# Performance work log

Measured on AMD Instinct MI355X. Metric: run time of the kernel, lower is better.

## Reference

```python
import jax, jax.numpy as jnp
import numpy as np

D_MODEL = 1024
NHEAD = 16
HEAD_DIM = D_MODEL // NHEAD


def setup_inputs() -> dict:
    key = jax.random.key(0)
    ks = jax.random.split(key, 9)
    B, T = 2, 2048
    s = 1.0 / np.sqrt(D_MODEL)
    return {
        "sequence": jax.random.normal(ks[0], (B, T, D_MODEL), dtype=jnp.float32),
        "wq": jax.random.normal(ks[1], (D_MODEL, D_MODEL), dtype=jnp.float32) * s,
        "bq": jax.random.normal(ks[2], (D_MODEL,), dtype=jnp.float32) * 0.01,
        "wk": jax.random.normal(ks[3], (D_MODEL, D_MODEL), dtype=jnp.float32) * s,
        "bk": jax.random.normal(ks[4], (D_MODEL,), dtype=jnp.float32) * 0.01,
        "wv": jax.random.normal(ks[5], (D_MODEL, D_MODEL), dtype=jnp.float32) * s,
        "bv": jax.random.normal(ks[6], (D_MODEL,), dtype=jnp.float32) * 0.01,
        "wo": jax.random.normal(ks[7], (D_MODEL, D_MODEL), dtype=jnp.float32) * s,
        "bo": jax.random.normal(ks[8], (D_MODEL,), dtype=jnp.float32) * 0.01,
    }


def reference(sequence, wq, bq, wk, bk, wv, bv, wo, bo):
    B, T, C = sequence.shape
    scale = jnp.asarray(HEAD_DIM ** 0.5, sequence.dtype)
    # projections (nn.Linear: x @ W.T + b)
    def proj(x, w, b):
        y = x @ w.T + b
        return y.reshape(B, T, NHEAD, HEAD_DIM).transpose(0, 2, 1, 3)  # [B,H,T,Dh]
    q = proj(sequence, wq, bq)
    k = proj(sequence, wk, bk)
    v = proj(sequence, wv, bv)
    scores = jnp.einsum("bhqd,bhkd->bhqk", q, k) / scale
    causal = jnp.tril(jnp.ones((T, T), dtype=bool))
    scores = jnp.where(causal, scores, jnp.asarray(-jnp.inf, scores.dtype))
    attn = jax.nn.softmax(scores, axis=-1)
    out = jnp.einsum("bhqk,bhkd->bhqd", attn, v)
    out = out.transpose(0, 2, 1, 3).reshape(B, T, C)
    return out @ wo.T + bo
```

## Files before the change

kernel.cpp:

```cpp
#include <hip/hip_runtime.h>
#include <hip/hip_bf16.h>
#include <hip/hip_fp16.h>
#include <type_traits>

#define DM 1024
#define NH 16
#define HD 64
#define BATCH 2
#define SEQ 2048
#define MROWS (BATCH*SEQ)

typedef __hip_bfloat16 bf16;
typedef __attribute__((ext_vector_type(8))) short    bf16x8;
typedef __attribute__((ext_vector_type(8))) short    s16x8;
typedef __attribute__((ext_vector_type(8))) _Float16 f16x8;
typedef __attribute__((ext_vector_type(4))) _Float16 f16x4;
typedef __attribute__((ext_vector_type(4))) short    s16x4;
typedef __attribute__((ext_vector_type(4))) float    f32x4;

#define LOG2E 1.44269504f
#define M_FIX 4.0f

__device__ __forceinline__ short f2bf(float x) {
    union { float f; unsigned u; } v; v.f = x;
    unsigned r = v.u + 0x7FFF + ((v.u >> 16) & 1);
    return (short)(r >> 16);
}

__device__ __forceinline__ bf16x8 ld8f(const float* p) {
    const float4 a = *(const float4*)p;
    const float4 b = *(const float4*)(p + 4);
    bf16x8 r;
    r[0]=f2bf(a.x); r[1]=f2bf(a.y); r[2]=f2bf(a.z); r[3]=f2bf(a.w);
    r[4]=f2bf(b.x); r[5]=f2bf(b.y); r[6]=f2bf(b.z); r[7]=f2bf(b.w);
    return r;
}

__device__ __forceinline__ void gload_lds16(const void* g, void* l) {
    __builtin_amdgcn_global_load_lds(
        (const __attribute__((address_space(1))) void*)g,
        (__attribute__((address_space(3))) void*)l, 16, 0, 0);
}

__global__ __launch_bounds__(256)
void cvt_bf16(const float* __restrict__ s0, const float* __restrict__ s1,
              const float* __restrict__ s2, const float* __restrict__ s3,
              const float* __restrict__ s4,
              short* d0, short* d1, short* d2, short* d3, short* d4)
{
    const int y = blockIdx.y;
    const float* src = (y==0? s0 : y==1? s1 : y==2? s2 : y==3? s3 : s4);
    short*       dst = (y==0? d0 : y==1? d1 : y==2? d2 : y==3? d3 : d4);
    const int n = (y == 0) ? MROWS*DM : DM*DM;
    const int i = (blockIdx.x * 256 + threadIdx.x) * 8;
    if (i < n) *(bf16x8*)(dst + i) = ld8f(src + i);
}

template<int MODE>
__device__ __forceinline__
void gemm_epilogue(f32x4 (&acc)[4][4], const float* bi, void* out, int z,
                   int tile_m, int tile_n, int wm, int wn,
                   int fr, int quad, int lane, short* lA)
{
    if (MODE == 1 && z == 2) {
        __syncthreads();
        short* sc = lA + (int)(threadIdx.x >> 6) * 256;
        const int rd = lane >> 2, tc = lane & 3;
        #pragma unroll
        for (int mi = 0; mi < 4; ++mi) {
            #pragma unroll
            for (int ni = 0; ni < 4; ++ni) {
                const int colg = tile_n + wn + ni*16 + fr;
                const float bia = bi[colg];
                f16x4 w;
                #pragma unroll
                for (int r = 0; r < 4; ++r) w[r] = (_Float16)(acc[mi][ni][r] + bia);
                *(f16x4*)(sc + fr*16 + quad*4) = w;
                const f16x4 vv = *(const f16x4*)(sc + rd*16 + tc*4);
                const int dg = tile_n + wn + ni*16 + rd;
                const int tg = tile_m + wm + mi*16 + tc*4;
                const int hh = dg >> 6, dd = dg & (HD-1);
                const int bb = tg >> 11, tt = tg & (SEQ-1);
                const int kt = tt >> 5, tko = tt & 31;
                *(f16x4*)((_Float16*)out +
                    ((((size_t)(bb*NH + hh))*(SEQ/32) + kt)*HD + dd)*32 + tko) = vv;
            }
        }
    } else {
        #pragma unroll
        for (int mi = 0; mi < 4; ++mi) {
            #pragma unroll
            for (int ni = 0; ni < 4; ++ni) {
                const int colg = tile_n + wn + ni*16 + fr;
                const float bia = bi[colg];
                #pragma unroll
                for (int r = 0; r < 4; ++r) {
                    const int rowg = tile_m + wm + mi*16 + quad*4 + r;
                    const float v = acc[mi][ni][r] + bia;
                    if (MODE == 0) {
                        ((float*)out)[(size_t)rowg*DM + colg] = v;
                    } else {
                        const int bb = rowg >> 11, t = rowg & (SEQ-1);
                        const int h  = colg >> 6,  d = colg & (HD-1);
                        ((_Float16*)out)[(((size_t)(bb*NH + h))*SEQ + t)*HD + d] = (_Float16)v;
                    }
                }
            }
        }
    }
}

template<int MODE>
__global__ __launch_bounds__(256)
void gemm_a(const short* __restrict__ A,
            const short* __restrict__ W0, const short* __restrict__ W1, const short* __restrict__ W2,
            const float* __restrict__ b0, const float* __restrict__ b1, const float* __restrict__ b2,
            void* o0, void* o1, void* o2)
{
    __shared__ __align__(16) short lA[128*32];
    __shared__ __align__(16) short lB[128*32];

    const int tid  = threadIdx.x;
    const int wid  = tid >> 6;
    const int lane = tid & 63;
    const int tile_n = blockIdx.x * 128;
    const int tile_m = blockIdx.y * 128;
    const int z = blockIdx.z;

    const short* Wg = (z == 0 ? W0 : (z == 1 ? W1 : W2));
    const float* bi = (z == 0 ? b0 : (z == 1 ? b1 : b2));
    void*        out = (z == 0 ? o0 : (z == 1 ? o1 : o2));

    const int sa_row = tile_m + wid*32 + (lane >> 2);
    const int sb_row = tile_n + wid*32 + (lane >> 2);
    const int scol   = (lane & 3) * 8;
    short* lA0 = lA + wid*1024 + lane*8;
    short* lA1 = lA0 + 512;
    short* lB0 = lB + wid*1024 + lane*8;
    short* lB1 = lB0 + 512;

    const int wm = (wid >> 1) * 64;
    const int wn = (wid & 1) * 64;
    const int fr = lane & 15;
    const int quad = lane >> 4;
    const int fq = quad * 8;

    f32x4 acc[4][4] = {};

    for (int k0 = 0; k0 < DM; k0 += 32) {
        __syncthreads();
        gload_lds16(A  + (size_t)sa_row*DM      + k0 + scol, lA0);
        gload_lds16(A  + (size_t)(sa_row+16)*DM + k0 + scol, lA1);
        gload_lds16(Wg + (size_t)sb_row*DM      + k0 + scol, lB0);
        gload_lds16(Wg + (size_t)(sb_row+16)*DM + k0 + scol, lB1);
        __syncthreads();

        bf16x8 af[4], bfv[4];
        #pragma unroll
        for (int i = 0; i < 4; ++i) af[i]  = *(const bf16x8*)(lA + (wm + i*16 + fr)*32 + fq);
        #pragma unroll
        for (int i = 0; i < 4; ++i) bfv[i] = *(const bf16x8*)(lB + (wn + i*16 + fr)*32 + fq);

        #pragma unroll
        for (int mi = 0; mi < 4; ++mi)
            #pragma unroll
            for (int ni = 0; ni < 4; ++ni)
                acc[mi][ni] = __builtin_amdgcn_mfma_f32_16x16x32_bf16(
                    af[mi], bfv[ni], acc[mi][ni], 0, 0, 0);
    }
    gemm_epilogue<MODE>(acc, bi, out, z, tile_m, tile_n, wm, wn, fr, quad, lane, lA);
}

template<typename TA, int MODE>
__global__ __launch_bounds__(256)
void gemm_f(const TA* __restrict__ A,
            const float* __restrict__ W0, const float* __restrict__ W1, const float* __restrict__ W2,
            const float* __restrict__ b0, const float* __restrict__ b1, const float* __restrict__ b2,
            void* o0, void* o1, void* o2)
{
    __shared__ __align__(16) short lA[128*32];
    __shared__ __align__(16) short lB[128*32];

    const int tid  = threadIdx.x;
    const int wid  = tid >> 6;
    const int lane = tid & 63;
    const int tile_n = blockIdx.x * 128;
    const int tile_m = blockIdx.y * 128;
    const int z = blockIdx.z;

    const float* Wg = (z == 0 ? W0 : (z == 1 ? W1 : W2));
    const float* bi = (z == 0 ? b0 : (z == 1 ? b1 : b2));
    void*        out = (z == 0 ? o0 : (z == 1 ? o1 : o2));

    const int sa_row = tile_m + wid*32 + (lane >> 2);
    const int sb_row = tile_n + wid*32 + (lane >> 2);
    const int scol   = (lane & 3) * 8;
    short* lA0 = lA + wid*1024 + lane*8;
    short* lA1 = lA0 + 512;
    short* lB0 = lB + wid*1024 + lane*8;
    short* lB1 = lB0 + 512;

    const int wm = (wid >> 1) * 64;
    const int wn = (wid & 1) * 64;
    const int fr = lane & 15;
    const int quad = lane >> 4;
    const int fq = quad * 8;

    f32x4 acc[4][4] = {};

    for (int k0 = 0; k0 < DM; k0 += 32) {
        bf16x8 ra0, ra1;
        if constexpr (std::is_same<TA, float>::value) {
            ra0 = ld8f((const float*)A + (size_t)sa_row*DM      + k0 + scol);
            ra1 = ld8f((const float*)A + (size_t)(sa_row+16)*DM + k0 + scol);
        } else {
            ra0 = *(const bf16x8*)((const short*)A + (size_t)sa_row*DM      + k0 + scol);
            ra1 = *(const bf16x8*)((const short*)A + (size_t)(sa_row+16)*DM + k0 + scol);
        }
        const bf16x8 rb0 = ld8f(Wg + (size_t)sb_row*DM      + k0 + scol);
        const bf16x8 rb1 = ld8f(Wg + (size_t)(sb_row+16)*DM + k0 + scol);

        __syncthreads();
        *(bf16x8*)lA0 = ra0;
        *(bf16x8*)lA1 = ra1;
        *(bf16x8*)lB0 = rb0;
        *(bf16x8*)lB1 = rb1;
        __syncthreads();

        bf16x8 af[4], bfv[4];
        #pragma unroll
        for (int i = 0; i < 4; ++i) af[i]  = *(const bf16x8*)(lA + (wm + i*16 + fr)*32 + fq);
        #pragma unroll
        for (int i = 0; i < 4; ++i) bfv[i] = *(const bf16x8*)(lB + (wn + i*16 + fr)*32 + fq);

        #pragma unroll
        for (int mi = 0; mi < 4; ++mi)
            #pragma unroll
            for (int ni = 0; ni < 4; ++ni)
                acc[mi][ni] = __builtin_amdgcn_mfma_f32_16x16x32_bf16(
                    af[mi], bfv[ni], acc[mi][ni], 0, 0, 0);
    }
    gemm_epilogue<MODE>(acc, bi, out, z, tile_m, tile_n, wm, wn, fr, quad, lane, lA);
}

__global__ __launch_bounds__(512)
void attn(const _Float16* __restrict__ Q, const _Float16* __restrict__ K,
          const _Float16* __restrict__ Vt, short* __restrict__ O)
{
    __shared__ __align__(16) _Float16 lsK[2][2][2048];
    __shared__ __align__(16) _Float16 lsV[2][2][2048];
    __shared__ __align__(16) float    comb[64*68];
    __shared__ float                  lcomb[64];

    const int t    = threadIdx.x;
    const int lane = t & 63;
    const int wid  = t >> 6;
    const int wg   = wid >> 2;
    const int widl = wid & 3;
    const int tg   = t & 255;
    const int id   = blockIdx.x;
    const int bh   = id & 31;
    const int xb   = id >> 5;
    const size_t base = (size_t)bh * SEQ * HD;
    const int qr = lane & 15;
    const int quad = lane >> 4;
    const int bb = bh >> 4, h = bh & (NH-1);

    const int k_goff = ((tg>>2)&31)*64 + (tg>>7)*32 + (tg&3)*8;
    const int v_goff = (tg&63)*32 + (tg>>6)*8;

    const float SC1 = 0.125f * LOG2E;
    const float SC2 = -M_FIX * LOG2E;
    const int vboff = (quad>>1)*512 + (quad&1)*4 + qr*8;

    #pragma unroll 1
    for (int half = 0; half < 2; ++half) {
        const int band = half ? (31 - xb) : xb;
        const int q_tile = band*64 + widl*16;
        const int q_idx  = q_tile + qr;
        const int nsub   = band + 1;
        const int k0sub  = wg * nsub;
        const int ktm    = 2*band + (widl >> 1);

        const f16x8* Qv = (const f16x8*)(Q + base + (size_t)q_idx*HD);
        const f16x8 qf0 = Qv[quad];
        const f16x8 qf1 = Qv[quad + 4];

        float l_cur = 0.f;
        f32x4 o[4] = {};

        gload_lds16(K  + base + (size_t)k0sub*2048 + k_goff, &lsK[wg][0][0] + tg*8);
        gload_lds16(Vt + base + (size_t)k0sub*2048 + v_goff, &lsV[wg][0][0] + tg*8);

        int cur = 0;
        #pragma unroll 1
        for (int u = 0; u < nsub; ++u) {
            if (u + 1 < nsub) {
                const size_t g = base + (size_t)(k0sub + u + 1)*2048;
                gload_lds16(K  + g + k_goff, &lsK[wg][cur^1][0] + tg*8);
                gload_lds16(Vt + g + v_goff, &lsV[wg][cur^1][0] + tg*8);
                asm volatile("s_waitcnt vmcnt(2)" ::: "memory");
            } else {
                asm volatile("s_waitcnt vmcnt(0)" ::: "memory");
            }
            __builtin_amdgcn_s_barrier();
            __builtin_amdgcn_sched_barrier(0);

            const int kt32 = k0sub + u;
            if (kt32 <= ktm) {
                const _Float16* sK = &lsK[wg][cur][0];
                const _Float16* sV = &lsV[wg][cur][0];

                const f16x8 ka0 = *(const f16x8*)(sK + qr*32 + quad*8);
                const f16x8 ka1 = *(const f16x8*)(sK + 1024 + qr*32 + quad*8);
                const f16x8 kb0 = *(const f16x8*)(sK + (16+qr)*32 + quad*8);
                const f16x8 kb1 = *(const f16x8*)(sK + 1024 + (16+qr)*32 + quad*8);

                __builtin_amdgcn_s_setprio(1);
                f32x4 s0 = {}, s1 = {};
                s0 = __builtin_amdgcn_mfma_f32_16x16x32_f16(ka0, qf0, s0, 0, 0, 0);
                s0 = __builtin_amdgcn_mfma_f32_16x16x32_f16(ka1, qf1, s0, 0, 0, 0);
                s1 = __builtin_amdgcn_mfma_f32_16x16x32_f16(kb0, qf0, s1, 0, 0, 0);
                s1 = __builtin_amdgcn_mfma_f32_16x16x32_f16(kb1, qf1, s1, 0, 0, 0);

                f16x4 p0, p1;
                const int k_base = kt32*32;
                if (kt32 == ktm) {
                    float ls = 0.f;
                    #pragma unroll
                    for (int r = 0; r < 4; ++r) {
                        const int key = k_base + quad*4 + r;
                        float e0 = exp2f(s0[r] * SC1 + SC2);
                        float e1 = exp2f(s1[r] * SC1 + SC2);
                        e0 = (key      <= q_idx) ? e0 : 0.f;
                        e1 = (key + 16 <= q_idx) ? e1 : 0.f;
                        ls += e0 + e1;
                        p0[r] = (_Float16)e0;
                        p1[r] = (_Float16)e1;
                    }
                    l_cur += ls;
                } else {
                    float ls = 0.f;
                    #pragma unroll
                    for (int r = 0; r < 4; ++r) {
                        const float e0 = exp2f(s0[r] * SC1 + SC2);
                        const float e1 = exp2f(s1[r] * SC1 + SC2);
                        ls += e0 + e1;
                        p0[r] = (_Float16)e0;
                        p1[r] = (_Float16)e1;
                    }
                    l_cur += ls;
                }

                #pragma unroll
                for (int dt = 0; dt < 4; ++dt) {
                    const f16x4 av0 = *(const f16x4*)(sV + vboff + dt*128);
                    const f16x4 av1 = *(const f16x4*)(sV + 1024 + vboff + dt*128);
                    o[dt] = __builtin_amdgcn_mfma_f32_16x16x16f16(av0, p0, o[dt], 0, 0, 0);
                    o[dt] = __builtin_amdgcn_mfma_f32_16x16x16f16(av1, p1, o[dt], 0, 0, 0);
                }
                __builtin_amdgcn_s_setprio(0);
            }
            __builtin_amdgcn_sched_barrier(0);
            __builtin_amdgcn_s_barrier();
            cur ^= 1;
        }

        l_cur += __shfl_xor(l_cur, 16, 64);
        l_cur += __shfl_xor(l_cur, 32, 64);

        if (wg == 1) {
            #pragma unroll
            for (int dt = 0; dt < 4; ++dt)
                *(f32x4*)&comb[(widl*16 + qr)*68 + dt*16 + quad*4] = o[dt];
            if (quad == 0) lcomb[widl*16 + qr] = l_cur;
        }
        __syncthreads();
        if (wg == 0) {
            const float ltot = l_cur + lcomb[widl*16 + qr];
            const float linv = 1.0f / fmaxf(ltot, 1e-30f);
            const int tq = q_tile + qr;
            #pragma unroll
            for (int dt = 0; dt < 4; ++dt) {
                const f32x4 o2 = *(const f32x4*)&comb[(widl*16 + qr)*68 + dt*16 + quad*4];
                s16x4 pk;
                #pragma unroll
                for (int r = 0; r < 4; ++r) pk[r] = f2bf((o[dt][r] + o2[r]) * linv);
                *(s16x4*)(O + ((size_t)(bb*SEQ + tq))*DM + h*HD + dt*16 + quad*4) = pk;
            }
        }
        __syncthreads();
    }
}

extern "C" void kernel_launch(void* const* d_in, const int* in_sizes, int n_in,
                              void* d_out, int out_size, void* d_ws, size_t ws_size,
                              hipStream_t stream)
{
    const float* seq = (const float*)d_in[0];
    const float* wq  = (const float*)d_in[1];
    const float* bq  = (const float*)d_in[2];
    const float* wk  = (const float*)d_in[3];
    const float* bk  = (const float*)d_in[4];
    const float* wv  = (const float*)d_in[5];
    const float* bv  = (const float*)d_in[6];
    const float* wo  = (const float*)d_in[7];
    const float* bo  = (const float*)d_in[8];

    _Float16* Qb = (_Float16*)d_ws;
    _Float16* Kb = Qb + (size_t)MROWS*DM;
    _Float16* Vt = Kb + (size_t)MROWS*DM;
    short*    Ob = (short*)(Vt + (size_t)MROWS*DM);
    short*    sq16 = Ob + (size_t)MROWS*DM;
    short*    wq16 = sq16 + (size_t)MROWS*DM;
    short*    wk16 = wq16 + (size_t)DM*DM;
    short*    wv16 = wk16 + (size_t)DM*DM;
    short*    wo16 = wv16 + (size_t)DM*DM;

    const size_t need = ((size_t)MROWS*DM*2)*5 + ((size_t)DM*DM*2)*4;
    const bool fast = ws_size >= need;

    if (fast) {
        dim3 gc(MROWS*DM/(256*8), 5, 1);
        cvt_bf16<<<gc, 256, 0, stream>>>(seq, wq, wk, wv, wo,
                                         sq16, wq16, wk16, wv16, wo16);

        dim3 g1(DM/128, MROWS/128, 3);
        gemm_a<1><<<g1, 256, 0, stream>>>(sq16, wq16, wk16, wv16, bq, bk, bv,
                                          (void*)Qb, (void*)Kb, (void*)Vt);

        attn<<<dim3(512), 512, 0, stream>>>(Qb, Kb, Vt, Ob);

        dim3 g3(DM/128, MROWS/128, 1);
        gemm_a<0><<<g3, 256, 0, stream>>>(Ob, wo16, wo16, wo16, bo, bo, bo,
                                          d_out, d_out, d_out);
    } else {
        dim3 g1(DM/128, MROWS/128, 3);
        gemm_f<float, 1><<<g1, 256, 0, stream>>>(seq, wq, wk, wv, bq, bk, bv,
                                                 (void*)Qb, (void*)Kb, (void*)Vt);

        attn<<<dim3(512), 512, 0, stream>>>(Qb, Kb, Vt, Ob);

        dim3 g3(DM/128, MROWS/128, 1);
        gemm_f<short, 0><<<g3, 256, 0, stream>>>(Ob, wo, wo, wo, bo, bo, bo,
                                                 d_out, d_out, d_out);
    }
}
```

Before: 188.6 us.

## Split attention KV range across four wave groups with interleaved subtiles

Doubles the attention block to 1024 threads so four wave groups each process every fourth 32-key subtile instead of two groups splitting contiguous halves. LDS is repacked into a single 64KB buffer reused for K/V double buffering and for a two-stage tree reduction of partial outputs and row sums. This shortens the serial key loop per wave to expose more parallelism. In exchange it adds extra barriers and reduction passes, and it may lower per-CU occupancy because of the larger block and LDS footprint.

```diff
diff --git a/kernel.cpp b/kernel.cpp
--- a/kernel.cpp
+++ b/kernel.cpp
@@ -243,14 +243,11 @@
     gemm_epilogue<MODE>(acc, bi, out, z, tile_m, tile_n, wm, wn, fr, quad, lane, lA);
 }
 
-__global__ __launch_bounds__(512)
+__global__ __launch_bounds__(1024, 8)
 void attn(const _Float16* __restrict__ Q, const _Float16* __restrict__ K,
           const _Float16* __restrict__ Vt, short* __restrict__ O)
 {
-    __shared__ __align__(16) _Float16 lsK[2][2][2048];
-    __shared__ __align__(16) _Float16 lsV[2][2][2048];
-    __shared__ __align__(16) float    comb[64*68];
-    __shared__ float                  lcomb[64];
+    __shared__ __align__(16) char smem[65536];
 
     const int t    = threadIdx.x;
     const int lane = t & 63;
@@ -266,20 +263,28 @@
     const int quad = lane >> 4;
     const int bb = bh >> 4, h = bh & (NH-1);
 
+    _Float16* lsK = (_Float16*)(smem + wg*16384);
+    _Float16* lsV = (_Float16*)(smem + wg*16384 + 8192);
+    float* comb0 = (float*)smem;
+    float* lc0   = (float*)(smem + 17408);
+    float* comb1 = (float*)(smem + 32768);
+    float* lc1   = (float*)(smem + 32768 + 17408);
+
     const int k_goff = ((tg>>2)&31)*64 + (tg>>7)*32 + (tg&3)*8;
     const int v_goff = (tg&63)*32 + (tg>>6)*8;
 
     const float SC1 = 0.125f * LOG2E;
     const float SC2 = -M_FIX * LOG2E;
     const int vboff = (quad>>1)*512 + (quad&1)*4 + qr*8;
+    const int row   = widl*16 + qr;
 
     #pragma unroll 1
     for (int half = 0; half < 2; ++half) {
         const int band = half ? (31 - xb) : xb;
         const int q_tile = band*64 + widl*16;
         const int q_idx  = q_tile + qr;
-        const int nsub   = band + 1;
-        const int k0sub  = wg * nsub;
+        const int nsubt  = 2*band + 2;
+        const int nsteps = (band >> 1) + 1;
         const int ktm    = 2*band + (widl >> 1);
 
         const f16x8* Qv = (const f16x8*)(Q + base + (size_t)q_idx*HD);
@@ -289,16 +294,19 @@
         float l_cur = 0.f;
         f32x4 o[4] = {};
 
-        gload_lds16(K  + base + (size_t)k0sub*2048 + k_goff, &lsK[wg][0][0] + tg*8);
-        gload_lds16(Vt + base + (size_t)k0sub*2048 + v_goff, &lsV[wg][0][0] + tg*8);
+        if (wg < nsubt) {
+            gload_lds16(K  + base + (size_t)wg*2048 + k_goff, lsK + tg*8);
+            gload_lds16(Vt + base + (size_t)wg*2048 + v_goff, lsV + tg*8);
+        }
 
         int cur = 0;
         #pragma unroll 1
-        for (int u = 0; u < nsub; ++u) {
-            if (u + 1 < nsub) {
-                const size_t g = base + (size_t)(k0sub + u + 1)*2048;
-                gload_lds16(K  + g + k_goff, &lsK[wg][cur^1][0] + tg*8);
-                gload_lds16(Vt + g + v_goff, &lsV[wg][cur^1][0] + tg*8);
+        for (int u = 0; u < nsteps; ++u) {
+            const int s = 4*u + wg;
+            if (s + 4 < nsubt) {
+                const size_t g = base + (size_t)(s + 4)*2048;
+                gload_lds16(K  + g + k_goff, lsK + (cur^1)*2048 + tg*8);
+                gload_lds16(Vt + g + v_goff, lsV + (cur^1)*2048 + tg*8);
                 asm volatile("s_waitcnt vmcnt(2)" ::: "memory");
             } else {
                 asm volatile("s_waitcnt vmcnt(0)" ::: "memory");
@@ -306,10 +314,9 @@
             __builtin_amdgcn_s_barrier();
             __builtin_amdgcn_sched_barrier(0);
 
-            const int kt32 = k0sub + u;
-            if (kt32 <= ktm) {
-                const _Float16* sK = &lsK[wg][cur][0];
-                const _Float16* sV = &lsV[wg][cur][0];
+            if (s <= ktm) {
+                const _Float16* sK = lsK + cur*2048;
+                const _Float16* sV = lsV + cur*2048;
 
                 const f16x8 ka0 = *(const f16x8*)(sK + qr*32 + quad*8);
                 const f16x8 ka1 = *(const f16x8*)(sK + 1024 + qr*32 + quad*8);
@@ -324,8 +331,8 @@
                 s1 = __builtin_amdgcn_mfma_f32_16x16x32_f16(kb1, qf1, s1, 0, 0, 0);
 
                 f16x4 p0, p1;
-                const int k_base = kt32*32;
-                if (kt32 == ktm) {
+                const int k_base = s*32;
+                if (s == ktm) {
                     float ls = 0.f;
                     #pragma unroll
                     for (int r = 0; r < 4; ++r) {
@@ -369,23 +376,49 @@
         l_cur += __shfl_xor(l_cur, 16, 64);
         l_cur += __shfl_xor(l_cur, 32, 64);
 
-        if (wg == 1) {
+        if (wg == 1 || wg == 3) {
+            float* cb = (wg == 1) ? comb0 : comb1;
+            float* lc = (wg == 1) ? lc0   : lc1;
             #pragma unroll
             for (int dt = 0; dt < 4; ++dt)
-                *(f32x4*)&comb[(widl*16 + qr)*68 + dt*16 + quad*4] = o[dt];
-            if (quad == 0) lcomb[widl*16 + qr] = l_cur;
+                *(f32x4*)&cb[row*68 + dt*16 + quad*4] = o[dt];
+            if (quad == 0) lc[row] = l_cur;
+        }
+        __syncthreads();
+        if (wg == 0 || wg == 2) {
+            const float* cb = (wg == 0) ? comb0 : comb1;
+            const float* lc = (wg == 0) ? lc0   : lc1;
+            #pragma unroll
+            for (int dt = 0; dt < 4; ++dt) {
+                const f32x4 o2 = *(const f32x4*)&cb[row*68 + dt*16 + quad*4];
+                #pragma unroll
+                for (int r = 0; r < 4; ++r) o[dt][r] += o2[r];
+            }
+            l_cur += lc[row];
+        }
+        __syncthreads();
+        if (wg == 2) {
+            #pragma unroll
+            for (int dt = 0; dt < 4; ++dt)
+                *(f32x4*)&comb1[row*68 + dt*16 + quad*4] = o[dt];
+            if (quad == 0) lc1[row] = l_cur;
         }
         __syncthreads();
         if (wg == 0) {
-            const float ltot = l_cur + lcomb[widl*16 + qr];
+            #pragma unroll
+            for (int dt = 0; dt < 4; ++dt) {
+                const f32x4 o2 = *(const f32x4*)&comb1[row*68 + dt*16 + quad*4];
+                #pragma unroll
+                for (int r = 0; r < 4; ++r) o[dt][r] += o2[r];
+            }
+            const float ltot = l_cur + lc1[row];
             const float linv = 1.0f / fmaxf(ltot, 1e-30f);
             const int tq = q_tile + qr;
             #pragma unroll
             for (int dt = 0; dt < 4; ++dt) {
-                const f32x4 o2 = *(const f32x4*)&comb[(widl*16 + qr)*68 + dt*16 + quad*4];
                 s16x4 pk;
                 #pragma unroll
-                for (int r = 0; r < 4; ++r) pk[r] = f2bf((o[dt][r] + o2[r]) * linv);
+                for (int r = 0; r < 4; ++r) pk[r] = f2bf(o[dt][r] * linv);
                 *(s16x4*)(O + ((size_t)(bb*SEQ + tq))*DM + h*HD + dt*16 + quad*4) = pk;
             }
         }
@@ -429,7 +462,7 @@
         gemm_a<1><<<g1, 256, 0, stream>>>(sq16, wq16, wk16, wv16, bq, bk, bv,
                                           (void*)Qb, (void*)Kb, (void*)Vt);
 
-        attn<<<dim3(512), 512, 0, stream>>>(Qb, Kb, Vt, Ob);
+        attn<<<dim3(512), 1024, 0, stream>>>(Qb, Kb, Vt, Ob);
 
         dim3 g3(DM/128, MROWS/128, 1);
         gemm_a<0><<<g3, 256, 0, stream>>>(Ob, wo16, wo16, wo16, bo, bo, bo,
@@ -439,7 +472,7 @@
         gemm_f<float, 1><<<g1, 256, 0, stream>>>(seq, wq, wk, wv, bq, bk, bv,
                                                  (void*)Qb, (void*)Kb, (void*)Vt);
 
-        attn<<<dim3(512), 512, 0, stream>>>(Qb, Kb, Vt, Ob);
+        attn<<<dim3(512), 1024, 0, stream>>>(Qb, Kb, Vt, Ob);
 
         dim3 g3(DM/128, MROWS/128, 1);
         gemm_f<short, 0><<<g3, 256, 0, stream>>>(Ob, wo, wo, wo, bo, bo, bo,
```

Result: slower. 211.4 us (+12.1%).
